# Kernel optimization log

Measured on AMD Instinct MI355X. Metric: run time of the kernel, lower is better.

The kernel has to match this reference:

```python
import jax, jax.numpy as jnp
import numpy as np

E, H, D = 64, 128, 2  # embedding_dim, hidden_dim, input_dim
PRED_LEN = 60


def lstm_cell(x, h, c, W_ih, W_hh, b_ih, b_hh):
    # PyTorch gate order: i, f, g, o
    gates = x @ W_ih.T + h @ W_hh.T + b_ih + b_hh  # (B, 4H)
    i, f, g, o = jnp.split(gates, 4, axis=-1)
    i = jax.nn.sigmoid(i)
    f = jax.nn.sigmoid(f)
    g = jnp.tanh(g)
    o = jax.nn.sigmoid(o)
    c = f * c + i * g
    h = o * jnp.tanh(c)
    return h, c


def setup_inputs() -> dict:
    key = jax.random.key(0)
    ks = jax.random.split(key, 12)
    B, T = 4096, 50
    s = lambda *sh: 1.0 / np.sqrt(sh[-1])
    inp = {
        "history": jax.random.normal(ks[0], (B, T, D), jnp.float32),
        "W_emb": jax.random.normal(ks[1], (E, D), jnp.float32) * s(E, D),
        "b_emb": jnp.zeros((E,), jnp.float32),
        "W_ih": jax.random.normal(ks[2], (4 * H, E), jnp.float32) * s(4 * H, E),
        "W_hh": jax.random.normal(ks[3], (4 * H, H), jnp.float32) * s(4 * H, H),
        "b_ih": jnp.zeros((4 * H,), jnp.float32),
        "b_hh": jnp.zeros((4 * H,), jnp.float32),
        "W1": jax.random.normal(ks[4], (H, H), jnp.float32) * s(H, H),
        "b1": jnp.zeros((H,), jnp.float32),
        "W2": jax.random.normal(ks[5], (D, H), jnp.float32) * s(D, H),
        "b2": jnp.zeros((D,), jnp.float32),
    }
    return inp


def reference(history, W_emb, b_emb, W_ih, W_hh, b_ih, b_hh, W1, b1, W2, b2):
    B = history.shape[0]
    # Input embedding for the whole history at once: (B, T, E)
    hist_embed = history @ W_emb.T + b_emb

    # --- Encoder LSTM over history ---
    h0 = jnp.zeros((B, H), history.dtype)
    c0 = jnp.zeros((B, H), history.dtype)

    def enc_step(carry, x_t):
        h, c = carry
        h, c = lstm_cell(x_t, h, c, W_ih, W_hh, b_ih, b_hh)
        return (h, c), None

    (h, c), _ = jax.lax.scan(enc_step, (h0, c0), jnp.swapaxes(hist_embed, 0, 1))

    prev = jnp.zeros((B, E), history.dtype)  # initial zero embedding

    def dec_step(carry, _):
        h, c, prev = carry
        h, c = lstm_cell(prev, h, c, W_ih, W_hh, b_ih, b_hh)
        hid = jax.nn.relu(h @ W1.T + b1)
        pred = hid @ W2.T + b2  # (B, D)
        prev = pred @ W_emb.T + b_emb
        return (h, c, prev), pred

    _, preds = jax.lax.scan(dec_step, (h, c, prev), None, length=PRED_LEN)
    return jnp.swapaxes(preds, 0, 1)  # (B, PRED_LEN, D)
```

## Files before the change

kernel.cpp:

```cpp
#include <hip/hip_runtime.h>
#include <math.h>

#define T_ENC 50
#define T_DEC 60
#define HID   128
#define EMB   64
#define DIN   2
#define MT    16
#define NTHR  512
#define HS    136

typedef __attribute__((ext_vector_type(8))) short frag8;
typedef __attribute__((ext_vector_type(4))) float f32x4;

__device__ __forceinline__ float fast_rcp(float x) { return __builtin_amdgcn_rcpf(x); }
__device__ __forceinline__ float sigm(float x) { return fast_rcp(1.f + __expf(-x)); }
__device__ __forceinline__ float tanh_fast(float x) { return fmaf(2.f, fast_rcp(1.f + __expf(-2.f * x)), -1.f); }

__device__ __forceinline__ void load_wfrag(const float* __restrict__ wrow,
                                           frag8& Fhi, frag8& Flo) {
    union { unsigned short s[8]; frag8 f; } hi, lo;
#pragma unroll
    for (int j = 0; j < 8; ++j) {
        float x      = wrow[j];
        unsigned u   = __float_as_uint(x);
        unsigned uhi = u & 0xffff0000u;
        float    lof = x - __uint_as_float(uhi);
        hi.s[j] = (unsigned short)(uhi >> 16);
        lo.s[j] = (unsigned short)(__float_as_uint(lof) >> 16);
    }
    Fhi = hi.f; Flo = lo.f;
}

__device__ __forceinline__ void split2(float x, unsigned short& hi, unsigned short& lo) {
    unsigned u   = __float_as_uint(x);
    unsigned uhi = u & 0xffff0000u;
    float    lof = x - __uint_as_float(uhi);
    hi = (unsigned short)(uhi >> 16);
    lo = (unsigned short)(__float_as_uint(lof) >> 16);
}

__global__ __launch_bounds__(NTHR, 2) void lstm_all(
    const float* __restrict__ history,
    const float* __restrict__ W_emb,
    const float* __restrict__ b_emb,
    const float* __restrict__ W_ih,
    const float* __restrict__ W_hh,
    const float* __restrict__ b_ih,
    const float* __restrict__ b_hh,
    const float* __restrict__ W1,
    const float* __restrict__ b1,
    const float* __restrict__ w2,
    const float* __restrict__ b2,
    float* __restrict__ out)
{
    __shared__ __align__(16) unsigned short hhi[MT * HS];
    __shared__ __align__(16) unsigned short hlo[MT * HS];
    __shared__ float hist_s[MT * T_ENC * DIN];
    __shared__ float2 part_s[8][MT];
    __shared__ float p_s[MT][DIN];
    __shared__ float wemb_s[EMB * DIN];
    __shared__ float bemb_s[EMB];

    const int tid = threadIdx.x;
    const int L   = tid & 63;
    const int w   = tid >> 6;
    const int nc  = L & 15;
    const int kb0 = (L >> 4) * 8;
    const int m0c = (L >> 4) * 4;
    const int r0  = blockIdx.x * MT;
    const int jcol = w * 16 + nc;

    for (int i = tid; i < MT * T_ENC * DIN; i += NTHR)
        hist_s[i] = history[r0 * T_ENC * DIN + i];
    for (int i = tid; i < MT * HS; i += NTHR) { hhi[i] = 0; hlo[i] = 0; }
    if (tid < EMB * DIN) wemb_s[tid] = W_emb[tid];
    if (tid < EMB) bemb_s[tid] = b_emb[tid];

    frag8 Bg[4][4][2];
#pragma unroll
    for (int g = 0; g < 4; ++g)
#pragma unroll
        for (int ks = 0; ks < 4; ++ks) {
            int n = g * HID + jcol;
            load_wfrag(&W_hh[(size_t)n * HID + ks * 32 + kb0], Bg[g][ks][0], Bg[g][ks][1]);
        }
    frag8 Bw1[4][2];
#pragma unroll
    for (int ks = 0; ks < 4; ++ks)
        load_wfrag(&W1[(size_t)jcol * HID + ks * 32 + kb0], Bw1[ks][0], Bw1[ks][1]);

    __syncthreads();

    float we0v[4], we1v[4], bs0v[4], bs1v[4];
#pragma unroll
    for (int g = 0; g < 4; ++g) {
        int n = g * HID + jcol;
        float s0 = 0.f, s1 = 0.f, sb = 0.f;
        const float* wr = &W_ih[(size_t)n * EMB];
#pragma unroll 4
        for (int e4 = 0; e4 < EMB / 4; ++e4) {
            float4 wv = *(const float4*)&wr[e4 * 4];
            int e = e4 * 4;
            s0 += wv.x * wemb_s[(e+0)*2] + wv.y * wemb_s[(e+1)*2]
                + wv.z * wemb_s[(e+2)*2] + wv.w * wemb_s[(e+3)*2];
            s1 += wv.x * wemb_s[(e+0)*2+1] + wv.y * wemb_s[(e+1)*2+1]
                + wv.z * wemb_s[(e+2)*2+1] + wv.w * wemb_s[(e+3)*2+1];
            sb += wv.x * bemb_s[e+0] + wv.y * bemb_s[e+1]
                + wv.z * bemb_s[e+2] + wv.w * bemb_s[e+3];
        }
        float b = b_ih[n] + b_hh[n];
        bs0v[g] = b;
        bs1v[g] = b + sb;
        we0v[g] = s0; we1v[g] = s1;
    }
    const float b1v  = b1[jcol];
    const float w2v0 = w2[jcol];
    const float w2v1 = w2[HID + jcol];
    const float b2v0 = b2[0], b2v1 = b2[1];
    const int   fb   = nc * HS + kb0;
    float cst[4] = {0.f, 0.f, 0.f, 0.f};

#pragma unroll 1
    for (int t = 0; t < T_ENC; ++t) {
        f32x4 acc[4];
        float q0[4], q1[4];
#pragma unroll
        for (int r = 0; r < 4; ++r) {
            float2 q = *(const float2*)&hist_s[(m0c + r) * (T_ENC * DIN) + t * DIN];
            q0[r] = q.x; q1[r] = q.y;
        }
#pragma unroll
        for (int g = 0; g < 4; ++g)
#pragma unroll
            for (int r = 0; r < 4; ++r)
                acc[g][r] = fmaf(q1[r], we1v[g], fmaf(q0[r], we0v[g], bs1v[g]));

#pragma unroll
        for (int ks = 0; ks < 4; ++ks) {
            frag8 Ahi = *(const frag8*)(hhi + fb + ks * 32);
            frag8 Alo = *(const frag8*)(hlo + fb + ks * 32);
#pragma unroll
            for (int g = 0; g < 4; ++g)
                acc[g] = __builtin_amdgcn_mfma_f32_16x16x32_bf16(Ahi, Bg[g][ks][1], acc[g], 0, 0, 0);
#pragma unroll
            for (int g = 0; g < 4; ++g)
                acc[g] = __builtin_amdgcn_mfma_f32_16x16x32_bf16(Alo, Bg[g][ks][0], acc[g], 0, 0, 0);
#pragma unroll
            for (int g = 0; g < 4; ++g)
                acc[g] = __builtin_amdgcn_mfma_f32_16x16x32_bf16(Ahi, Bg[g][ks][0], acc[g], 0, 0, 0);
        }
        __syncthreads();

#pragma unroll
        for (int r = 0; r < 4; ++r) {
            float i_ = sigm(acc[0][r]);
            float f_ = sigm(acc[1][r]);
            float gv = tanh_fast(acc[2][r]);
            float o_ = sigm(acc[3][r]);
            cst[r] = fmaf(f_, cst[r], i_ * gv);
            float h = o_ * tanh_fast(cst[r]);
            unsigned short phi, plo;
            split2(h, phi, plo);
            hhi[(m0c + r) * HS + jcol] = phi;
            hlo[(m0c + r) * HS + jcol] = plo;
        }
        __syncthreads();
    }

#pragma unroll 1
    for (int it = 0; it < T_DEC; ++it) {
        f32x4 acc[4];
        f32x4 hacc;
#pragma unroll
        for (int g = 0; g < 4; ++g) {
            float b = (it == 0) ? bs0v[g] : bs1v[g];
            acc[g] = (f32x4){b, b, b, b};
        }
        hacc = (f32x4){b1v, b1v, b1v, b1v};

        if (it == 0) {
#pragma unroll
            for (int ks = 0; ks < 4; ++ks) {
                frag8 Ahi = *(const frag8*)(hhi + fb + ks * 32);
                frag8 Alo = *(const frag8*)(hlo + fb + ks * 32);
#pragma unroll
                for (int g = 0; g < 4; ++g)
                    acc[g] = __builtin_amdgcn_mfma_f32_16x16x32_bf16(Ahi, Bg[g][ks][1], acc[g], 0, 0, 0);
#pragma unroll
                for (int g = 0; g < 4; ++g)
                    acc[g] = __builtin_amdgcn_mfma_f32_16x16x32_bf16(Alo, Bg[g][ks][0], acc[g], 0, 0, 0);
#pragma unroll
                for (int g = 0; g < 4; ++g)
                    acc[g] = __builtin_amdgcn_mfma_f32_16x16x32_bf16(Ahi, Bg[g][ks][0], acc[g], 0, 0, 0);
            }
            __syncthreads();
        } else {
#pragma unroll
            for (int ks = 0; ks < 4; ++ks) {
                frag8 Ahi = *(const frag8*)(hhi + fb + ks * 32);
                frag8 Alo = *(const frag8*)(hlo + fb + ks * 32);
#pragma unroll
                for (int g = 0; g < 4; ++g)
                    acc[g] = __builtin_amdgcn_mfma_f32_16x16x32_bf16(Ahi, Bg[g][ks][1], acc[g], 0, 0, 0);
                hacc = __builtin_amdgcn_mfma_f32_16x16x32_bf16(Ahi, Bw1[ks][1], hacc, 0, 0, 0);
#pragma unroll
                for (int g = 0; g < 4; ++g)
                    acc[g] = __builtin_amdgcn_mfma_f32_16x16x32_bf16(Alo, Bg[g][ks][0], acc[g], 0, 0, 0);
                hacc = __builtin_amdgcn_mfma_f32_16x16x32_bf16(Alo, Bw1[ks][0], hacc, 0, 0, 0);
#pragma unroll
                for (int g = 0; g < 4; ++g)
                    acc[g] = __builtin_amdgcn_mfma_f32_16x16x32_bf16(Ahi, Bg[g][ks][0], acc[g], 0, 0, 0);
                hacc = __builtin_amdgcn_mfma_f32_16x16x32_bf16(Ahi, Bw1[ks][0], hacc, 0, 0, 0);
            }

            float p0[4], p1[4];
#pragma unroll
            for (int r = 0; r < 4; ++r) {
                float hv = fmaxf(hacc[r], 0.f);
                p0[r] = hv * w2v0;
                p1[r] = hv * w2v1;
            }
#pragma unroll
            for (int mask = 1; mask < 16; mask <<= 1)
#pragma unroll
                for (int r = 0; r < 4; ++r) {
                    p0[r] += __shfl_xor(p0[r], mask);
                    p1[r] += __shfl_xor(p1[r], mask);
                }
            if (nc == 0)
#pragma unroll
                for (int r = 0; r < 4; ++r)
                    part_s[w][m0c + r] = (float2){p0[r], p1[r]};
            __syncthreads();

            if (tid < 32) {
                int m = tid >> 1, d = tid & 1;
                float s = (d == 0) ? b2v0 : b2v1;
#pragma unroll
                for (int wi = 0; wi < 8; ++wi) {
                    float2 v = part_s[wi][m];
                    s += (d == 0) ? v.x : v.y;
                }
                out[((size_t)(r0 + m) * T_DEC + (it - 1)) * DIN + d] = s;
                p_s[m][d] = s;
            }
            __syncthreads();

            float q0[4], q1[4];
#pragma unroll
            for (int r = 0; r < 4; ++r) { q0[r] = p_s[m0c + r][0]; q1[r] = p_s[m0c + r][1]; }
#pragma unroll
            for (int g = 0; g < 4; ++g)
#pragma unroll
                for (int r = 0; r < 4; ++r)
                    acc[g][r] += fmaf(q1[r], we1v[g], q0[r] * we0v[g]);
        }

#pragma unroll
        for (int r = 0; r < 4; ++r) {
            float i_ = sigm(acc[0][r]);
            float f_ = sigm(acc[1][r]);
            float gv = tanh_fast(acc[2][r]);
            float o_ = sigm(acc[3][r]);
            cst[r] = fmaf(f_, cst[r], i_ * gv);
            float h = o_ * tanh_fast(cst[r]);
            unsigned short phi, plo;
            split2(h, phi, plo);
            hhi[(m0c + r) * HS + jcol] = phi;
            hlo[(m0c + r) * HS + jcol] = plo;
        }
        __syncthreads();
    }

    {
        f32x4 hacc = (f32x4){b1v, b1v, b1v, b1v};
#pragma unroll
        for (int ks = 0; ks < 4; ++ks) {
            frag8 Ahi = *(const frag8*)(hhi + fb + ks * 32);
            frag8 Alo = *(const frag8*)(hlo + fb + ks * 32);
            hacc = __builtin_amdgcn_mfma_f32_16x16x32_bf16(Ahi, Bw1[ks][1], hacc, 0, 0, 0);
            hacc = __builtin_amdgcn_mfma_f32_16x16x32_bf16(Alo, Bw1[ks][0], hacc, 0, 0, 0);
            hacc = __builtin_amdgcn_mfma_f32_16x16x32_bf16(Ahi, Bw1[ks][0], hacc, 0, 0, 0);
        }
        float p0[4], p1[4];
#pragma unroll
        for (int r = 0; r < 4; ++r) {
            float hv = fmaxf(hacc[r], 0.f);
            p0[r] = hv * w2v0;
            p1[r] = hv * w2v1;
        }
#pragma unroll
        for (int mask = 1; mask < 16; mask <<= 1)
#pragma unroll
            for (int r = 0; r < 4; ++r) {
                p0[r] += __shfl_xor(p0[r], mask);
                p1[r] += __shfl_xor(p1[r], mask);
            }
        if (nc == 0)
#pragma unroll
            for (int r = 0; r < 4; ++r)
                part_s[w][m0c + r] = (float2){p0[r], p1[r]};
        __syncthreads();
        if (tid < 32) {
            int m = tid >> 1, d = tid & 1;
            float s = (d == 0) ? b2v0 : b2v1;
#pragma unroll
            for (int wi = 0; wi < 8; ++wi) {
                float2 v = part_s[wi][m];
                s += (d == 0) ? v.x : v.y;
            }
            out[((size_t)(r0 + m) * T_DEC + (T_DEC - 1)) * DIN + d] = s;
        }
    }
}

extern "C" void kernel_launch(void* const* d_in, const int* in_sizes, int n_in,
                              void* d_out, int out_size, void* d_ws, size_t ws_size,
                              hipStream_t stream) {
    const float* history = (const float*)d_in[0];
    const float* W_emb   = (const float*)d_in[1];
    const float* b_emb   = (const float*)d_in[2];
    const float* W_ih    = (const float*)d_in[3];
    const float* W_hh    = (const float*)d_in[4];
    const float* b_ih    = (const float*)d_in[5];
    const float* b_hh    = (const float*)d_in[6];
    const float* W1      = (const float*)d_in[7];
    const float* b1      = (const float*)d_in[8];
    const float* W2      = (const float*)d_in[9];
    const float* b2      = (const float*)d_in[10];
    float* out = (float*)d_out;
    (void)d_ws; (void)ws_size; (void)in_sizes; (void)n_in; (void)out_size;

    lstm_all<<<4096 / MT, NTHR, 0, stream>>>(history, W_emb, b_emb, W_ih, W_hh,
                                             b_ih, b_hh, W1, b1, W2, b2, out);
}
```

Baseline: 357.3 us.

## Double-buffer hidden state to drop a barrier per step; stage predictions in LDS

The shared hidden-state split buffers become ping-pong pairs, so each recurrent step reads one buffer and writes the other. This removes the __syncthreads that separated the MFMA reads from the state writes in both the encoder and decoder loops. Decoder predictions are kept in an LDS buffer and written to global memory in one coalesced pass at the end, instead of scattered per-step stores. The cost is extra LDS (two state buffers plus the prediction buffer), which may affect occupancy at two blocks per CU.

```diff
diff --git a/kernel.cpp b/kernel.cpp
--- a/kernel.cpp
+++ b/kernel.cpp
@@ -54,11 +54,11 @@
     const float* __restrict__ b2,
     float* __restrict__ out)
 {
-    __shared__ __align__(16) unsigned short hhi[MT * HS];
-    __shared__ __align__(16) unsigned short hlo[MT * HS];
+    __shared__ __align__(16) unsigned short hhi[2][MT * HS];
+    __shared__ __align__(16) unsigned short hlo[2][MT * HS];
     __shared__ float hist_s[MT * T_ENC * DIN];
+    __shared__ float pred_buf[MT * T_DEC * DIN];
     __shared__ float2 part_s[8][MT];
-    __shared__ float p_s[MT][DIN];
     __shared__ float wemb_s[EMB * DIN];
     __shared__ float bemb_s[EMB];
 
@@ -73,7 +73,10 @@
 
     for (int i = tid; i < MT * T_ENC * DIN; i += NTHR)
         hist_s[i] = history[r0 * T_ENC * DIN + i];
-    for (int i = tid; i < MT * HS; i += NTHR) { hhi[i] = 0; hlo[i] = 0; }
+    for (int i = tid; i < MT * HS; i += NTHR) {
+        hhi[0][i] = 0; hlo[0][i] = 0;
+        hhi[1][i] = 0; hlo[1][i] = 0;
+    }
     if (tid < EMB * DIN) wemb_s[tid] = W_emb[tid];
     if (tid < EMB) bemb_s[tid] = b_emb[tid];
 
@@ -120,6 +123,7 @@
     const float b2v0 = b2[0], b2v1 = b2[1];
     const int   fb   = nc * HS + kb0;
     float cst[4] = {0.f, 0.f, 0.f, 0.f};
+    int pb = 0;
 
 #pragma unroll 1
     for (int t = 0; t < T_ENC; ++t) {
@@ -136,10 +140,12 @@
             for (int r = 0; r < 4; ++r)
                 acc[g][r] = fmaf(q1[r], we1v[g], fmaf(q0[r], we0v[g], bs1v[g]));
 
+        const unsigned short* Hh = hhi[pb];
+        const unsigned short* Hl = hlo[pb];
 #pragma unroll
         for (int ks = 0; ks < 4; ++ks) {
-            frag8 Ahi = *(const frag8*)(hhi + fb + ks * 32);
-            frag8 Alo = *(const frag8*)(hlo + fb + ks * 32);
+            frag8 Ahi = *(const frag8*)(Hh + fb + ks * 32);
+            frag8 Alo = *(const frag8*)(Hl + fb + ks * 32);
 #pragma unroll
             for (int g = 0; g < 4; ++g)
                 acc[g] = __builtin_amdgcn_mfma_f32_16x16x32_bf16(Ahi, Bg[g][ks][1], acc[g], 0, 0, 0);
@@ -150,8 +156,8 @@
             for (int g = 0; g < 4; ++g)
                 acc[g] = __builtin_amdgcn_mfma_f32_16x16x32_bf16(Ahi, Bg[g][ks][0], acc[g], 0, 0, 0);
         }
-        __syncthreads();
-
+
+        const int nb = pb ^ 1;
 #pragma unroll
         for (int r = 0; r < 4; ++r) {
             float i_ = sigm(acc[0][r]);
@@ -162,28 +168,30 @@
             float h = o_ * tanh_fast(cst[r]);
             unsigned short phi, plo;
             split2(h, phi, plo);
-            hhi[(m0c + r) * HS + jcol] = phi;
-            hlo[(m0c + r) * HS + jcol] = plo;
-        }
+            hhi[nb][(m0c + r) * HS + jcol] = phi;
+            hlo[nb][(m0c + r) * HS + jcol] = plo;
+        }
+        pb = nb;
         __syncthreads();
     }
 
 #pragma unroll 1
     for (int it = 0; it < T_DEC; ++it) {
         f32x4 acc[4];
-        f32x4 hacc;
+        f32x4 hacc = (f32x4){b1v, b1v, b1v, b1v};
 #pragma unroll
         for (int g = 0; g < 4; ++g) {
             float b = (it == 0) ? bs0v[g] : bs1v[g];
             acc[g] = (f32x4){b, b, b, b};
         }
-        hacc = (f32x4){b1v, b1v, b1v, b1v};
-
+
+        const unsigned short* Hh = hhi[pb];
+        const unsigned short* Hl = hlo[pb];
         if (it == 0) {
 #pragma unroll
             for (int ks = 0; ks < 4; ++ks) {
-                frag8 Ahi = *(const frag8*)(hhi + fb + ks * 32);
-                frag8 Alo = *(const frag8*)(hlo + fb + ks * 32);
+                frag8 Ahi = *(const frag8*)(Hh + fb + ks * 32);
+                frag8 Alo = *(const frag8*)(Hl + fb + ks * 32);
 #pragma unroll
                 for (int g = 0; g < 4; ++g)
                     acc[g] = __builtin_amdgcn_mfma_f32_16x16x32_bf16(Ahi, Bg[g][ks][1], acc[g], 0, 0, 0);
@@ -194,12 +202,11 @@
                 for (int g = 0; g < 4; ++g)
                     acc[g] = __builtin_amdgcn_mfma_f32_16x16x32_bf16(Ahi, Bg[g][ks][0], acc[g], 0, 0, 0);
             }
-            __syncthreads();
         } else {
 #pragma unroll
             for (int ks = 0; ks < 4; ++ks) {
-                frag8 Ahi = *(const frag8*)(hhi + fb + ks * 32);
-                frag8 Alo = *(const frag8*)(hlo + fb + ks * 32);
+                frag8 Ahi = *(const frag8*)(Hh + fb + ks * 32);
+                frag8 Alo = *(const frag8*)(Hl + fb + ks * 32);
 #pragma unroll
                 for (int g = 0; g < 4; ++g)
                     acc[g] = __builtin_amdgcn_mfma_f32_16x16x32_bf16(Ahi, Bg[g][ks][1], acc[g], 0, 0, 0);
@@ -242,21 +249,20 @@
                     float2 v = part_s[wi][m];
                     s += (d == 0) ? v.x : v.y;
                 }
-                out[((size_t)(r0 + m) * T_DEC + (it - 1)) * DIN + d] = s;
-                p_s[m][d] = s;
+                pred_buf[(m * T_DEC + (it - 1)) * DIN + d] = s;
             }
             __syncthreads();
 
-            float q0[4], q1[4];
-#pragma unroll
-            for (int r = 0; r < 4; ++r) { q0[r] = p_s[m0c + r][0]; q1[r] = p_s[m0c + r][1]; }
-#pragma unroll
-            for (int g = 0; g < 4; ++g)
-#pragma unroll
-                for (int r = 0; r < 4; ++r)
-                    acc[g][r] += fmaf(q1[r], we1v[g], q0[r] * we0v[g]);
-        }
-
+#pragma unroll
+            for (int r = 0; r < 4; ++r) {
+                float2 pq = *(const float2*)&pred_buf[((m0c + r) * T_DEC + (it - 1)) * DIN];
+#pragma unroll
+                for (int g = 0; g < 4; ++g)
+                    acc[g][r] += fmaf(pq.y, we1v[g], pq.x * we0v[g]);
+            }
+        }
+
+        const int nb = pb ^ 1;
 #pragma unroll
         for (int r = 0; r < 4; ++r) {
             float i_ = sigm(acc[0][r]);
@@ -267,18 +273,21 @@
             float h = o_ * tanh_fast(cst[r]);
             unsigned short phi, plo;
             split2(h, phi, plo);
-            hhi[(m0c + r) * HS + jcol] = phi;
-            hlo[(m0c + r) * HS + jcol] = plo;
-        }
+            hhi[nb][(m0c + r) * HS + jcol] = phi;
+            hlo[nb][(m0c + r) * HS + jcol] = plo;
+        }
+        pb = nb;
         __syncthreads();
     }
 
     {
         f32x4 hacc = (f32x4){b1v, b1v, b1v, b1v};
+        const unsigned short* Hh = hhi[pb];
+        const unsigned short* Hl = hlo[pb];
 #pragma unroll
         for (int ks = 0; ks < 4; ++ks) {
-            frag8 Ahi = *(const frag8*)(hhi + fb + ks * 32);
-            frag8 Alo = *(const frag8*)(hlo + fb + ks * 32);
+            frag8 Ahi = *(const frag8*)(Hh + fb + ks * 32);
+            frag8 Alo = *(const frag8*)(Hl + fb + ks * 32);
             hacc = __builtin_amdgcn_mfma_f32_16x16x32_bf16(Ahi, Bw1[ks][1], hacc, 0, 0, 0);
             hacc = __builtin_amdgcn_mfma_f32_16x16x32_bf16(Alo, Bw1[ks][0], hacc, 0, 0, 0);
             hacc = __builtin_amdgcn_mfma_f32_16x16x32_bf16(Ahi, Bw1[ks][0], hacc, 0, 0, 0);
@@ -310,9 +319,13 @@
                 float2 v = part_s[wi][m];
                 s += (d == 0) ? v.x : v.y;
             }
-            out[((size_t)(r0 + m) * T_DEC + (T_DEC - 1)) * DIN + d] = s;
-        }
-    }
+            pred_buf[(m * T_DEC + (T_DEC - 1)) * DIN + d] = s;
+        }
+        __syncthreads();
+    }
+
+    for (int i = tid; i < MT * T_DEC * DIN; i += NTHR)
+        out[(size_t)r0 * T_DEC * DIN + i] = pred_buf[i];
 }
 
 extern "C" void kernel_launch(void* const* d_in, const int* in_sizes, int n_in,
```

After: 353.0 us. About the same (-1.2%).
